# Performance work log

Hardware: AMD Instinct MI355X
Metric: run time of the kernel (lower is better)

## Reference

```python
import jax, jax.numpy as jnp
import numpy as np

MASS, CHARGE, ALPHA, BETA = 1.0, 0.5, 0.1, 0.05
ETA = jnp.array([1.0, -1.0, -1.0, -1.0], dtype=jnp.float32)  # Minkowski metric diag


def setup_inputs() -> dict:
    key = jax.random.key(0)
    k1, k2, k3 = jax.random.split(key, 3)
    B = 262144
    y = jax.random.normal(k1, (B, 8), dtype=jnp.float32)
    W = jax.random.normal(k2, (4, 4), dtype=jnp.float32) * 0.3
    V = jax.random.normal(k3, (4, 4), dtype=jnp.float32) * 0.3
    return {"y": y, "W": W, "V": V}


def _lagrangian(z):
    # z = (x, u, A) concatenated, shape [12]
    x, u, A = z[0:4], z[4:8], z[8:12]
    kinetic = 0.5 * MASS * jnp.sum(ETA * u * u)
    coupling = CHARGE * jnp.sum(ETA * u * A)
    xu_term = ALPHA * jnp.sum((x * u) ** 2)      # makes J_xu nontrivial
    uA_term = BETA * jnp.sum(u * A) ** 2          # makes J_Au nontrivial
    return kinetic + coupling + xu_term + uA_term


def reference(y, W, V):
    def A_vec(x):  # vector potential A^mu(x), works on [4] or [B,4]
        return jnp.tanh(x @ W.T) + x @ V.T

    x = y[:, 0:4]   # [B,4] positions
    u = y[:, 4:8]   # [B,4] velocities
    A = A_vec(x)    # [B,4]
    z = jnp.concatenate([x, u, A], axis=1)  # [B,12] = (x,u,A)

    gradL = jax.vmap(jax.grad(_lagrangian))(z)      # [B,12]
    H = jax.vmap(jax.hessian(_lagrangian))(z)       # [B,12,12]

    dL_dx = gradL[:, 0:4]
    dL_dA = gradL[:, 8:12]
    J_xu = H[:, 0:4, 4:8]    # d^2L/(dx^mu du^nu)
    J_uu = H[:, 4:8, 4:8]    # d^2L/(du^mu du^nu)
    J_Au = H[:, 8:12, 4:8]   # d^2L/(dA^mu du^nu)

    # dA_dx[a, nu, i] = dA^i/dx^nu (matches tf.stack(..., axis=2) layout)
    jacA = jax.vmap(jax.jacfwd(A_vec))(x)           # [B, i, nu]
    dA_dx = jnp.transpose(jacA, (0, 2, 1))          # [B, nu, i]

    J_uu_inv = jnp.linalg.pinv(J_uu)                # [B,4,4]

    force = (dL_dx
             + jnp.einsum('ajk,ak->aj', dA_dx, dL_dA)
             - jnp.einsum('ai,aij->aj', u,
                          J_xu + jnp.einsum('ajk,akm->ajm', dA_dx, J_Au)))
    acceleration = jnp.einsum('ai,aij->aj', force, J_uu_inv)  # [B,4]
    return acceleration
```

## Files before the change

kernel.cpp:

```cpp
#include <hip/hip_runtime.h>
#include <math.h>


#define SIX_RCOND 2.86102294921875e-5
#define RCOND     4.76837158203125e-6

__device__ __forceinline__ float rcp_nr(float x) {
    float r = __builtin_amdgcn_rcpf(x);
    r = r * (2.0f - x * r);
    return r;
}

__device__ __forceinline__ void fast_tanh4(const double t[4], double th[4])
{
    const double LOG2E = 1.4426950408889634074;
    const double LN2HI = 6.93147180369123816490e-01;
    const double LN2LO = 1.90821492927058770002e-10;
    double e[4], opp[4];
    #pragma unroll
    for (int j = 0; j < 4; ++j) {
        double a  = fabs(t[j]);
        double z  = -2.0 * a;
        double zc = fmax(z, -64.0);
        double nf = rint(zc * LOG2E);
        double r  = fma(-nf, LN2HI, zc);
        r = fma(-nf, LN2LO, r);
        double p = 2.75573192239858906526e-07;
        p = fma(p, r, 2.75573192239858925110e-06);
        p = fma(p, r, 2.48015873015873015873e-05);
        p = fma(p, r, 1.98412698412698412698e-04);
        p = fma(p, r, 1.38888888888888888889e-03);
        p = fma(p, r, 8.33333333333333333333e-03);
        p = fma(p, r, 4.16666666666666666667e-02);
        p = fma(p, r, 1.66666666666666666667e-01);
        p = fma(p, r, 0.5);
        p = fma(p, r, 1.0);
        p = fma(p, r, 1.0);
        int n = (int)nf;
        double twon = __longlong_as_double(((long long)(1023 + n)) << 52);
        double ez = p * twon;
        ez = (z <= -40.0) ? 0.0 : ez;
        e[j]   = ez;
        opp[j] = 1.0 + ez;
    }
    double p01 = opp[0] * opp[1], p23 = opp[2] * opp[3];
    double rp  = 1.0 / (p01 * p23);
    double inv[4] = { opp[1] * p23 * rp, opp[0] * p23 * rp,
                      p01 * opp[3] * rp, p01 * opp[2] * rp };
    #pragma unroll
    for (int j = 0; j < 4; ++j)
        th[j] = copysign((1.0 - e[j]) * inv[j], t[j]);
}

__device__ __forceinline__ void model_terms_f64(
    const double* sW, const double* sV,
    const double x[4], const double u[4],
    double A[4], double f[4], double d[4])
{
    const double eta[4] = {1.0, -1.0, -1.0, -1.0};
    const double CHG = 0.5, ALPHA = 0.1, BETA = 0.05;
    double t[4], s[4];
    #pragma unroll
    for (int j = 0; j < 4; ++j) {
        double tj = 0.0, sj = 0.0;
        #pragma unroll
        for (int k = 0; k < 4; ++k) {
            tj = fma(sW[j*4+k], x[k], tj);
            sj = fma(sV[j*4+k], x[k], sj);
        }
        t[j] = tj; s[j] = sj;
    }
    double th[4];
    fast_tanh4(t, th);
    double G[4][4];
    #pragma unroll
    for (int j = 0; j < 4; ++j) {
        A[j] = th[j] + s[j];
        double dth = 1.0 - th[j] * th[j];
        #pragma unroll
        for (int k = 0; k < 4; ++k) G[j][k] = fma(dth, sW[j*4+k], sV[j*4+k]);
    }
    double S = 0.0;
    #pragma unroll
    for (int k = 0; k < 4; ++k) S += u[k] * A[k];
    double P[4], R[4], Q[4];
    #pragma unroll
    for (int j = 0; j < 4; ++j) {
        double p = 0.0, r = 0.0, q = 0.0;
        #pragma unroll
        for (int k = 0; k < 4; ++k) {
            p += G[k][j] * u[k];
            r += G[j][k] * u[k];
            q += G[k][j] * (CHG * eta[k]) * u[k];
        }
        P[j] = p; R[j] = r; Q[j] = q;
    }
    double T = 0.0;
    #pragma unroll
    for (int j = 0; j < 4; ++j) T += u[j] * R[j];
    #pragma unroll
    for (int j = 0; j < 4; ++j) {
        f[j] = -2.0 * ALPHA * x[j] * u[j] * u[j]
             + Q[j]
             + 2.0 * BETA * S * P[j]
             - (CHG * eta[j] + 2.0 * BETA * S) * R[j]
             - 2.0 * BETA * A[j] * T;
        d[j] = eta[j] + 2.0 * ALPHA * x[j] * x[j];
    }
}

__device__ __forceinline__ void sm_solve_f64(
    const double d[4], const double A[4], const double f[4], double acc[4])
{
    const double C2 = 0.1;
    double b[4], fd[4], den = 1.0, w = 0.0;
    #pragma unroll
    for (int j = 0; j < 4; ++j) {
        double inv = 1.0 / d[j];
        b[j]  = A[j] * inv;
        fd[j] = f[j] * inv;
        den  += C2 * A[j] * b[j];
        w    += b[j] * f[j];
    }
    double scale = C2 * w / den;
    #pragma unroll
    for (int j = 0; j < 4; ++j) acc[j] = fd[j] - b[j] * scale;
}

__device__ __forceinline__ bool criterion_f64(
    const double d[4], const double A[4])
{
    const double C2 = 0.1;
    double mind = 1e300;
    #pragma unroll
    for (int j = 0; j < 4; ++j) {
        double a = fabs(d[j]);
        mind = (a < mind) ? a : mind;
    }
    double p01 = d[0] * d[1], p23 = d[2] * d[3];
    double det = p01 * p23
        + C2 * (A[0]*A[0]*(d[1]*p23) + A[1]*A[1]*(d[0]*p23) +
                A[2]*A[2]*(p01*d[3]) + A[3]*A[3]*(p01*d[2]));
    double sumA2 = 0.0, sumA4 = 0.0, F2 = 0.0;
    #pragma unroll
    for (int j = 0; j < 4; ++j) {
        double Aj2 = A[j] * A[j];
        sumA2 += Aj2; sumA4 += Aj2 * Aj2;
        double Jjj = d[j] + C2 * Aj2;
        F2 += Jjj * Jjj;
    }
    F2 += C2 * C2 * (sumA2 * sumA2 - sumA4);
    double rowmax = 0.0;
    #pragma unroll
    for (int r = 0; r < 4; ++r) {
        double rs = 0.0;
        #pragma unroll
        for (int c = 0; c < 4; ++c) {
            double Jrc = C2 * A[r] * A[c] + ((r == c) ? d[r] : 0.0);
            rs += fabs(Jrc);
        }
        rowmax = (rs > rowmax) ? rs : rowmax;
    }
    double sig_hi2 = rowmax * rowmax;
    sig_hi2 = (F2 < sig_hi2) ? F2 : sig_hi2;
    return (fabs(det) > SIX_RCOND * sig_hi2 * sig_hi2) && (mind > 1e-3);
}

__device__ __forceinline__ void jacobi_pinv_reg(
    const double d[4], const double A[4], const double f[4], double acc[4])
{
    const double C2 = 0.1;
    double M[4][4], Vm[4][4];
    #pragma unroll
    for (int r = 0; r < 4; ++r) {
        #pragma unroll
        for (int c = 0; c < 4; ++c) {
            M[r][c] = C2 * A[r] * A[c];
            Vm[r][c] = (r == c) ? 1.0 : 0.0;
        }
        M[r][r] += d[r];
    }
    for (int sweep = 0; sweep < 6; ++sweep) {
        #pragma unroll
        for (int p = 0; p < 3; ++p) {
            #pragma unroll
            for (int q2 = p + 1; q2 < 4; ++q2) {
                double apq = M[p][q2];
                bool active = fabs(apq) > 1e-280;
                double div = active ? (2.0 * apq) : 1.0;
                double tau = (M[q2][q2] - M[p][p]) / div;
                double tt = ((tau >= 0.0) ? 1.0 : -1.0) /
                            (fabs(tau) + sqrt(1.0 + tau * tau));
                double c = 1.0 / sqrt(1.0 + tt * tt);
                double s = tt * c;
                c = active ? c : 1.0;
                s = active ? s : 0.0;
                #pragma unroll
                for (int k = 0; k < 4; ++k) {
                    double mkp = M[k][p], mkq = M[k][q2];
                    M[k][p]  = c * mkp - s * mkq;
                    M[k][q2] = s * mkp + c * mkq;
                }
                #pragma unroll
                for (int k = 0; k < 4; ++k) {
                    double mpk = M[p][k], mqk = M[q2][k];
                    M[p][k]  = c * mpk - s * mqk;
                    M[q2][k] = s * mpk + c * mqk;
                }
                #pragma unroll
                for (int k = 0; k < 4; ++k) {
                    double vkp = Vm[k][p], vkq = Vm[k][q2];
                    Vm[k][p]  = c * vkp - s * vkq;
                    Vm[k][q2] = s * vkp + c * vkq;
                }
            }
        }
    }
    double lam[4], sigmax = 0.0;
    #pragma unroll
    for (int k = 0; k < 4; ++k) {
        lam[k] = M[k][k];
        double a = fabs(lam[k]);
        sigmax = (a > sigmax) ? a : sigmax;
    }
    double cutoff = RCOND * sigmax;
    #pragma unroll
    for (int j = 0; j < 4; ++j) acc[j] = 0.0;
    #pragma unroll
    for (int e = 0; e < 4; ++e) {
        double coef = 0.0;
        #pragma unroll
        for (int k = 0; k < 4; ++k) coef += Vm[k][e] * f[k];
        coef /= lam[e];
        coef = (fabs(lam[e]) > cutoff) ? coef : 0.0;
        #pragma unroll
        for (int j = 0; j < 4; ++j) acc[j] += coef * Vm[j][e];
    }
}

__global__ __launch_bounds__(256, 2) void fused_kernel(
    const float* __restrict__ y, const float* __restrict__ W,
    const float* __restrict__ V, float* __restrict__ out,
    unsigned int* __restrict__ cnt, double* __restrict__ data,
    int* __restrict__ idxs, unsigned int cap, int B)
{
    __shared__ float  sW[16],  sV[16];
    __shared__ double sWd[16], sVd[16];
    __shared__ int sList[256];
    __shared__ int sCount;

    if (threadIdx.x == 0) sCount = 0;
    if (threadIdx.x < 16) {
        float w = W[threadIdx.x];
        sW[threadIdx.x]  = w;
        sWd[threadIdx.x] = (double)w;
    } else if (threadIdx.x < 32) {
        float v = V[threadIdx.x - 16];
        sV[threadIdx.x - 16]  = v;
        sVd[threadIdx.x - 16] = (double)v;
    }
    __syncthreads();

    int i = blockIdx.x * blockDim.x + threadIdx.x;
    const float4* y4 = (const float4*)y;

    if (i < B) {
        float4 xv = y4[2 * i];
        float4 uv = y4[2 * i + 1];
        float x[4] = {xv.x, xv.y, xv.z, xv.w};
        float u[4] = {uv.x, uv.y, uv.z, uv.w};

        const float eta[4] = {1.0f, -1.0f, -1.0f, -1.0f};
        const float CHG = 0.5f, ALPHA = 0.1f, BETA = 0.05f, C2 = 0.1f;
        const float NEG2LOG2E = -2.8853900817779268f;

        float t[4], sv[4];
        #pragma unroll
        for (int j = 0; j < 4; ++j) {
            float tj = 0.0f, sj = 0.0f;
            #pragma unroll
            for (int k = 0; k < 4; ++k) {
                tj = fmaf(sW[j*4+k], x[k], tj);
                sj = fmaf(sV[j*4+k], x[k], sj);
            }
            t[j] = tj; sv[j] = sj;
        }
        float A[4], dth[4];
        #pragma unroll
        for (int j = 0; j < 4; ++j) {
            float a  = fabsf(t[j]);
            float e  = __builtin_amdgcn_exp2f(a * NEG2LOG2E);
            float th = copysignf((1.0f - e) * rcp_nr(1.0f + e), t[j]);
            A[j]   = th + sv[j];
            dth[j] = 1.0f - th * th;
        }
        float G[4][4];
        #pragma unroll
        for (int j = 0; j < 4; ++j)
            #pragma unroll
            for (int k = 0; k < 4; ++k)
                G[j][k] = fmaf(dth[j], sW[j*4+k], sV[j*4+k]);

        float S = 0.0f;
        #pragma unroll
        for (int k = 0; k < 4; ++k) S = fmaf(u[k], A[k], S);
        float P[4], R[4], Q[4];
        #pragma unroll
        for (int j = 0; j < 4; ++j) {
            float p = 0.0f, r = 0.0f, q = 0.0f;
            #pragma unroll
            for (int k = 0; k < 4; ++k) {
                p = fmaf(G[k][j], u[k], p);
                r = fmaf(G[j][k], u[k], r);
                q = fmaf(G[k][j] * (CHG * eta[k]), u[k], q);
            }
            P[j] = p; R[j] = r; Q[j] = q;
        }
        float T = 0.0f;
        #pragma unroll
        for (int j = 0; j < 4; ++j) T = fmaf(u[j], R[j], T);
        float f[4], d[4];
        #pragma unroll
        for (int j = 0; j < 4; ++j) {
            f[j] = -2.0f * ALPHA * x[j] * u[j] * u[j]
                 + Q[j]
                 + 2.0f * BETA * S * P[j]
                 - (CHG * eta[j] + 2.0f * BETA * S) * R[j]
                 - 2.0f * BETA * A[j] * T;
            d[j] = eta[j] + 2.0f * ALPHA * x[j] * x[j];
        }

        float mind = fminf(fminf(fabsf(d[0]), fabsf(d[1])),
                           fminf(fabsf(d[2]), fabsf(d[3])));
        float p01 = d[0] * d[1], p23 = d[2] * d[3];
        float prod = p01 * p23;
        float det = prod
            + C2 * (A[0]*A[0]*(d[1]*p23) + A[1]*A[1]*(d[0]*p23) +
                    A[2]*A[2]*(p01*d[3]) + A[3]*A[3]*(p01*d[2]));
        float rowmax = 0.0f;
        #pragma unroll
        for (int r = 0; r < 4; ++r) {
            float rs = 0.0f;
            #pragma unroll
            for (int c = 0; c < 4; ++c) {
                float Jrc = C2 * A[r] * A[c] + ((r == c) ? d[r] : 0.0f);
                rs += fabsf(Jrc);
            }
            rowmax = fmaxf(rs, rowmax);
        }
        float sig2 = rowmax * rowmax;
        bool safe = (fabsf(det) > sig2 * sig2 * (1.0f / 1024.0f)) && (mind > 1e-3f);

        if (safe) {
            float invprod = rcp_nr(prod);
            float invd[4] = { d[1] * p23 * invprod, d[0] * p23 * invprod,
                              p01 * d[3] * invprod, p01 * d[2] * invprod };
            float b[4], fd[4], den = 1.0f, w = 0.0f;
            #pragma unroll
            for (int j = 0; j < 4; ++j) {
                b[j]  = A[j] * invd[j];
                fd[j] = f[j] * invd[j];
                den   = fmaf(C2 * A[j], b[j], den);
                w     = fmaf(b[j], f[j], w);
            }
            float scale = (C2 * w) * rcp_nr(den);
            float4 res;
            res.x = fd[0] - b[0] * scale; res.y = fd[1] - b[1] * scale;
            res.z = fd[2] - b[2] * scale; res.w = fd[3] - b[3] * scale;
            ((float4*)out)[i] = res;
        } else {
            int k = atomicAdd(&sCount, 1);
            sList[k] = i;
        }
    }
    __syncthreads();

    int nd = sCount;
    if ((int)threadIdx.x < nd) {
        int ii = sList[threadIdx.x];
        float4 xv = y4[2 * ii];
        float4 uv = y4[2 * ii + 1];
        double x[4] = {xv.x, xv.y, xv.z, xv.w};
        double u[4] = {uv.x, uv.y, uv.z, uv.w};
        double A[4], f[4], d[4];
        model_terms_f64(sWd, sVd, x, u, A, f, d);

        bool safe64 = criterion_f64(d, A);
        bool deferred = false;
        if (!safe64) {
            unsigned int idx = atomicAdd(cnt, 1u);
            if (idx < cap) {
                double* rec = data + (size_t)idx * 12;
                #pragma unroll
                for (int j = 0; j < 4; ++j) rec[j]     = A[j];
                #pragma unroll
                for (int j = 0; j < 4; ++j) rec[4 + j] = f[j];
                #pragma unroll
                for (int j = 0; j < 4; ++j) rec[8 + j] = d[j];
                idxs[idx] = ii;
                deferred = true;
            }
        }
        if (!deferred) {
            double acc[4];
            sm_solve_f64(d, A, f, acc);
            float4 res;
            res.x = (float)acc[0]; res.y = (float)acc[1];
            res.z = (float)acc[2]; res.w = (float)acc[3];
            ((float4*)out)[ii] = res;
        }
    }
}

__global__ __launch_bounds__(64, 1) void slow_kernel(
    float* __restrict__ out,
    const unsigned int* __restrict__ cnt, const double* __restrict__ data,
    const int* __restrict__ idxs, unsigned int cap)
{
    unsigned int n = *cnt;
    if (n > cap) n = cap;
    int stride = gridDim.x * blockDim.x;
    for (unsigned int j = blockIdx.x * blockDim.x + threadIdx.x; j < n; j += stride) {
        const double* rec = data + (size_t)j * 12;
        double A[4], f[4], d[4];
        #pragma unroll
        for (int k = 0; k < 4; ++k) A[k] = rec[k];
        #pragma unroll
        for (int k = 0; k < 4; ++k) f[k] = rec[4 + k];
        #pragma unroll
        for (int k = 0; k < 4; ++k) d[k] = rec[8 + k];
        int i = idxs[j];

        double acc[4];
        jacobi_pinv_reg(d, A, f, acc);

        float4 res;
        res.x = (float)acc[0]; res.y = (float)acc[1];
        res.z = (float)acc[2]; res.w = (float)acc[3];
        ((float4*)out)[i] = res;
    }
}

extern "C" void kernel_launch(void* const* d_in, const int* in_sizes, int n_in,
                              void* d_out, int out_size, void* d_ws, size_t ws_size,
                              hipStream_t stream) {
    const float* y = (const float*)d_in[0];
    const float* W = (const float*)d_in[1];
    const float* V = (const float*)d_in[2];
    float* out = (float*)d_out;
    int B = in_sizes[0] / 8;

    unsigned int* cnt = (unsigned int*)d_ws;
    unsigned int cap = 0;
    if (ws_size > 16) {
        size_t avail = ws_size - 16;
        cap = (unsigned int)(avail / (12 * sizeof(double) + sizeof(int)));
    }
    if (cap > (unsigned int)B) cap = (unsigned int)B;
    double* data = (double*)((char*)d_ws + 16);
    int* idxs = (int*)((char*)d_ws + 16 + (size_t)cap * 12 * sizeof(double));

    hipMemsetAsync(d_ws, 0, 16, stream);

    int block = 256;
    int grid = (B + block - 1) / block;
    fused_kernel<<<grid, block, 0, stream>>>(y, W, V, out, cnt, data, idxs, cap, B);
    slow_kernel<<<128, 64, 0, stream>>>(out, cnt, data, idxs, cap);
}
```

Before: 78.95 us.

## Use per-block deferred-work slots instead of a global atomic counter

Deferred hard cases are now counted with a shared-memory atomic in each block and written into that block's own slot region, with a per-block count array. This replaces the single global atomic counter, and because every block writes its count unconditionally, the hipMemsetAsync that reset the counter is no longer needed. The slow kernel now launches one 64-thread block per fused block and reads that block's list. The intent is to remove global atomic contention and one extra launch. In exchange it needs much more workspace, and per-block capacity shrinks when the workspace is small, so more cases may fall back to the fused-path solve. It also launches many slow-kernel blocks that mostly have no work.

Result: slower. 98.65 us (+24.9%).

```diff
diff --git a/kernel.cpp b/kernel.cpp
--- a/kernel.cpp
+++ b/kernel.cpp
@@ -241,15 +241,16 @@
 __global__ __launch_bounds__(256, 2) void fused_kernel(
     const float* __restrict__ y, const float* __restrict__ W,
     const float* __restrict__ V, float* __restrict__ out,
-    unsigned int* __restrict__ cnt, double* __restrict__ data,
-    int* __restrict__ idxs, unsigned int cap, int B)
+    int* __restrict__ cntArr, double* __restrict__ data,
+    int* __restrict__ idxs, unsigned int capPB, int B)
 {
     __shared__ float  sW[16],  sV[16];
     __shared__ double sWd[16], sVd[16];
     __shared__ int sList[256];
     __shared__ int sCount;
-
-    if (threadIdx.x == 0) sCount = 0;
+    __shared__ int sCount2;
+
+    if (threadIdx.x == 0) { sCount = 0; sCount2 = 0; }
     if (threadIdx.x < 16) {
         float w = W[threadIdx.x];
         sW[threadIdx.x]  = w;
@@ -388,16 +389,17 @@
         bool safe64 = criterion_f64(d, A);
         bool deferred = false;
         if (!safe64) {
-            unsigned int idx = atomicAdd(cnt, 1u);
-            if (idx < cap) {
-                double* rec = data + (size_t)idx * 12;
+            int slot = atomicAdd(&sCount2, 1);
+            if ((unsigned int)slot < capPB) {
+                size_t rbase = (size_t)blockIdx.x * capPB + (unsigned int)slot;
+                double* rec = data + rbase * 12;
                 #pragma unroll
                 for (int j = 0; j < 4; ++j) rec[j]     = A[j];
                 #pragma unroll
                 for (int j = 0; j < 4; ++j) rec[4 + j] = f[j];
                 #pragma unroll
                 for (int j = 0; j < 4; ++j) rec[8 + j] = d[j];
-                idxs[idx] = ii;
+                idxs[rbase] = ii;
                 deferred = true;
             }
         }
@@ -410,18 +412,22 @@
             ((float4*)out)[ii] = res;
         }
     }
+    __syncthreads();
+    if (threadIdx.x == 0) {
+        int c2 = sCount2;
+        cntArr[blockIdx.x] = (c2 < (int)capPB) ? c2 : (int)capPB;
+    }
 }
 
 __global__ __launch_bounds__(64, 1) void slow_kernel(
     float* __restrict__ out,
-    const unsigned int* __restrict__ cnt, const double* __restrict__ data,
-    const int* __restrict__ idxs, unsigned int cap)
-{
-    unsigned int n = *cnt;
-    if (n > cap) n = cap;
-    int stride = gridDim.x * blockDim.x;
-    for (unsigned int j = blockIdx.x * blockDim.x + threadIdx.x; j < n; j += stride) {
-        const double* rec = data + (size_t)j * 12;
+    const int* __restrict__ cntArr, const double* __restrict__ data,
+    const int* __restrict__ idxs, unsigned int capPB)
+{
+    int n = cntArr[blockIdx.x];
+    for (int j = (int)threadIdx.x; j < n; j += 64) {
+        size_t rbase = (size_t)blockIdx.x * capPB + (unsigned int)j;
+        const double* rec = data + rbase * 12;
         double A[4], f[4], d[4];
         #pragma unroll
         for (int k = 0; k < 4; ++k) A[k] = rec[k];
@@ -429,7 +435,7 @@
         for (int k = 0; k < 4; ++k) f[k] = rec[4 + k];
         #pragma unroll
         for (int k = 0; k < 4; ++k) d[k] = rec[8 + k];
-        int i = idxs[j];
+        int i = idxs[rbase];
 
         double acc[4];
         jacobi_pinv_reg(d, A, f, acc);
@@ -450,20 +456,26 @@
     float* out = (float*)d_out;
     int B = in_sizes[0] / 8;
 
-    unsigned int* cnt = (unsigned int*)d_ws;
-    unsigned int cap = 0;
-    if (ws_size > 16) {
-        size_t avail = ws_size - 16;
-        cap = (unsigned int)(avail / (12 * sizeof(double) + sizeof(int)));
-    }
-    if (cap > (unsigned int)B) cap = (unsigned int)B;
-    double* data = (double*)((char*)d_ws + 16);
-    int* idxs = (int*)((char*)d_ws + 16 + (size_t)cap * 12 * sizeof(double));
-
-    hipMemsetAsync(d_ws, 0, 16, stream);
-
     int block = 256;
     int grid = (B + block - 1) / block;
-    fused_kernel<<<grid, block, 0, stream>>>(y, W, V, out, cnt, data, idxs, cap, B);
-    slow_kernel<<<128, 64, 0, stream>>>(out, cnt, data, idxs, cap);
-}
+
+    unsigned int capPB = 256;
+    size_t cntBytes = (size_t)grid * sizeof(int);
+    size_t need = [&](unsigned int c) {
+        return ((cntBytes + 7) & ~(size_t)7) +
+               (size_t)grid * c * (12 * sizeof(double) + sizeof(int));
+    }(capPB);
+    while (capPB > 0 && need > ws_size) {
+        capPB >>= 1;
+        need = ((cntBytes + 7) & ~(size_t)7) +
+               (size_t)grid * capPB * (12 * sizeof(double) + sizeof(int));
+    }
+    int* cntArr = (int*)d_ws;
+    char* p = (char*)d_ws + ((cntBytes + 7) & ~(size_t)7);
+    double* data = (double*)p;
+    int* idxs = (int*)(p + (size_t)grid * capPB * 12 * sizeof(double));
+
+    fused_kernel<<<grid, block, 0, stream>>>(y, W, V, out, cntArr, data, idxs,
+                                             capPB, B);
+    slow_kernel<<<grid, 64, 0, stream>>>(out, cntArr, data, idxs, capPB);
+}
```
